# Optimization experiments

Measured on AMD Instinct MI355X. Metric: run time of the kernel, lower is better.

The kernel has to match this reference:

```python
import jax, jax.numpy as jnp
import numpy as np

EPS = 1e-5      # F.layer_norm default eps
ALPHA = 0.08    # ALALLaDA blend coefficient


def setup_inputs() -> dict:
    key = jax.random.key(0)
    ks = jax.random.split(key, 6)
    B, S, D, K = 2, 2048, 2048, 8
    Fh = D // 4
    h_L = jax.random.normal(ks[0], (B, S, D), jnp.float32)
    # nonzero -> masked position (stands in for input_ids == 126336)
    mask = jax.random.randint(ks[1], (B, S), 0, 2).astype(jnp.int32)
    Wr = jax.random.normal(ks[2], (K, D), jnp.float32) / np.sqrt(D).astype(np.float32)
    br = jnp.zeros((K,), jnp.float32)
    W1 = jax.random.normal(ks[3], (K, D, Fh), jnp.float32) / np.sqrt(D).astype(np.float32)
    b1 = jnp.zeros((K, Fh), jnp.float32)
    W2 = jax.random.normal(ks[4], (K, Fh, D), jnp.float32) / np.sqrt(Fh).astype(np.float32)
    b2 = jnp.zeros((K, D), jnp.float32)
    return {"h_L": h_L, "mask": mask, "Wr": Wr, "br": br,
            "W1": W1, "b1": b1, "W2": W2, "b2": b2, "range_r": 8}


def _router_blend(h_L, Wr, br, W1, b1, W2, b2, mask, range_r):
    B, S, D = h_L.shape
    masked = mask != 0
    um = (~masked).astype(h_L.dtype)  # unmasked validity [B,S]
    # Per-token, per-expert outputs M[b,s,k,d]: Linear -> exact GELU -> Linear.
    pre = jnp.einsum('bsd,kdf->bskf', h_L, W1) + b1
    M = jnp.einsum('bskf,kfd->bskd', jax.nn.gelu(pre, approximate=False), W2) + b2
    # Routing weights at every position (softmax over K experts).
    w = jax.nn.softmax(jnp.einsum('bsd,kd->bsk', h_L, Wr) + br, axis=-1)
    # Accumulate weighted expert outputs over the +/-range_r neighbor window,
    # counting only unmasked neighbors. Fixed small loop over 2r offsets.
    num = jnp.zeros((B, S, D), h_L.dtype)
    cnt = jnp.zeros((B, S), h_L.dtype)
    for o in range(-range_r, range_r + 1):
        if o == 0:
            continue
        if o > 0:  # neighbor t = a + o: shift left, zero-pad tail
            Mo = jnp.pad(M[:, o:], ((0, 0), (0, o), (0, 0), (0, 0)))
            vo = jnp.pad(um[:, o:], ((0, 0), (0, o)))
        else:      # neighbor t = a + o (o<0): shift right, zero-pad head
            Mo = jnp.pad(M[:, :o], ((0, 0), (-o, 0), (0, 0), (0, 0)))
            vo = jnp.pad(um[:, :o], ((0, 0), (-o, 0)))
        num = num + vo[..., None] * jnp.einsum('bsk,bskd->bsd', w, Mo)
        cnt = cnt + vo
    has = cnt > 0
    mean = num / jnp.maximum(cnt, 1.0)[..., None]   # mean over valid neighbors
    # layer_norm over d_model, no affine
    mu = mean.mean(-1, keepdims=True)
    var = jnp.mean((mean - mu) ** 2, axis=-1, keepdims=True)
    ln = (mean - mu) / jnp.sqrt(var + EPS)
    # delta is written only at masked positions that had >=1 neighbor
    delta = jnp.where((masked & has)[..., None], ln, 0.0)
    return h_L + ALPHA * delta


def reference(h_L, mask, Wr, br, W1, b1, W2, b2, range_r):
    return _router_blend(h_L, Wr, br, W1, b1, W2, b2, mask, range_r)
```

## Files before the change

### kernel.cpp

```cpp
#include <hip/hip_runtime.h>
#include <hip/hip_bf16.h>
#include <math.h>


#define ALPHA 0.08f
#define EPS 1e-5f

typedef __attribute__((ext_vector_type(8))) __bf16 bf16x8;
typedef __attribute__((ext_vector_type(8))) short short8;
typedef __attribute__((ext_vector_type(4))) float f32x4;

__device__ __forceinline__ unsigned short f2bf(float f) {
  unsigned u = __float_as_uint(f);
  u += 0x7fffu + ((u >> 16) & 1u);
  return (unsigned short)(u >> 16);
}
__device__ __forceinline__ float bf2f(unsigned short b) {
  return __uint_as_float(((unsigned)b) << 16);
}

#define GLD16(gptr, lptr)                                                     \
  __builtin_amdgcn_global_load_lds(                                           \
      (const __attribute__((address_space(1))) void*)(gptr),                  \
      (__attribute__((address_space(3))) void*)(lptr), 16, 0, 0)

__device__ __forceinline__ int wave_incl_scan(int v, int lane) {
#pragma unroll
  for (int off = 1; off < 64; off <<= 1) {
    int t = __shfl_up(v, off);
    if (lane >= off) v += t;
  }
  return v;
}

__global__ __launch_bounds__(1024) void scan_kernel(
    const int* __restrict__ mask, const int* __restrict__ rptr,
    int* __restrict__ ru, int* __restrict__ unm_idx,
    int* __restrict__ msk_idx, int* __restrict__ pos2row,
    int* __restrict__ counts) {
  __shared__ int sru[4097];
  __shared__ int wsum[16];
  __shared__ int wsum2[17];
  const int tid = threadIdx.x;
  const int lane = tid & 63, wv = tid >> 6;
  const int t0 = tid * 4;
  const int4 m4 = *(const int4*)(mask + t0);
  int f[4];
  f[0] = (m4.x == 0); f[1] = (m4.y == 0); f[2] = (m4.z == 0); f[3] = (m4.w == 0);
  const int tsum = f[0] + f[1] + f[2] + f[3];
  const int isc = wave_incl_scan(tsum, lane);
  if (lane == 63) wsum[wv] = isc;
  __syncthreads();
  if (tid == 0) {
    int acc = 0;
#pragma unroll
    for (int i = 0; i < 16; ++i) { int v = wsum[i]; wsum[i] = acc; acc += v; }
    sru[4096] = acc;
    counts[0] = acc;
    ru[4096] = acc;
  }
  __syncthreads();
  int ex = wsum[wv] + isc - tsum;
#pragma unroll
  for (int j = 0; j < 4; ++j) {
    sru[t0 + j] = ex;
    ru[t0 + j] = ex;
    if (f[j]) unm_idx[ex] = t0 + j;
    ex += f[j];
  }
  __syncthreads();
  const int r = rptr[0];
  int mval[4] = {m4.x, m4.y, m4.z, m4.w};
  int g[4];
#pragma unroll
  for (int j = 0; j < 4; ++j) {
    const int t = t0 + j;
    const int s = t & 2047, tb = t & ~2047;
    const int lo = max(s - r, 0), hi = min(s + r, 2047);
    const int cnt = sru[tb + hi + 1] - sru[tb + lo];
    g[j] = (mval[j] != 0 && cnt > 0) ? 1 : 0;
  }
  const int tsum2 = g[0] + g[1] + g[2] + g[3];
  const int isc2 = wave_incl_scan(tsum2, lane);
  if (lane == 63) wsum2[wv] = isc2;
  __syncthreads();
  if (tid == 0) {
    int acc = 0;
#pragma unroll
    for (int i = 0; i < 16; ++i) { int v = wsum2[i]; wsum2[i] = acc; acc += v; }
    counts[1] = acc;
  }
  __syncthreads();
  int ex2 = wsum2[wv] + isc2 - tsum2;
#pragma unroll
  for (int j = 0; j < 4; ++j) {
    const int t = t0 + j;
    pos2row[t] = g[j] ? ex2 : -1;
    if (g[j]) msk_idx[ex2] = t;
    ex2 += g[j];
  }
}

__global__ void packrouter_kernel(const float* __restrict__ h,
                                  const int* __restrict__ mask,
                                  const int* __restrict__ ru,
                                  const float* __restrict__ Wr,
                                  const float* __restrict__ br,
                                  float* __restrict__ w,
                                  unsigned short* __restrict__ hbc) {
  const int a = blockIdx.x;
  const int tid = threadIdx.x;
  const int lane = tid & 63, wid = tid >> 6;
  const size_t base = (size_t)a * 2048;
  const int d0 = tid * 8;
  float hv[8];
  *(float4*)(hv) = *(const float4*)(h + base + d0);
  *(float4*)(hv + 4) = *(const float4*)(h + base + d0 + 4);
  float acc[8];
#pragma unroll
  for (int k = 0; k < 8; ++k) {
    float wvv[8];
    *(float4*)(wvv) = *(const float4*)(Wr + (size_t)k * 2048 + d0);
    *(float4*)(wvv + 4) = *(const float4*)(Wr + (size_t)k * 2048 + d0 + 4);
    float s = 0.f;
#pragma unroll
    for (int j = 0; j < 8; ++j) s += hv[j] * wvv[j];
    acc[k] = s;
  }
#pragma unroll
  for (int off = 32; off > 0; off >>= 1)
#pragma unroll
    for (int k = 0; k < 8; ++k) acc[k] += __shfl_down(acc[k], off);
  __shared__ float red[4][8];
  __shared__ float logits[8];
  if (lane == 0)
#pragma unroll
    for (int k = 0; k < 8; ++k) red[wid][k] = acc[k];
  __syncthreads();
  if (tid < 8)
    logits[tid] = red[0][tid] + red[1][tid] + red[2][tid] + red[3][tid] + br[tid];
  __syncthreads();
  if (tid == 0) {
    float mx = logits[0];
#pragma unroll
    for (int k = 1; k < 8; ++k) mx = fmaxf(mx, logits[k]);
    float e[8], se = 0.f;
#pragma unroll
    for (int k = 0; k < 8; ++k) {
      e[k] = expf(logits[k] - mx);
      se += e[k];
    }
    const float is = 1.f / se;
#pragma unroll
    for (int k = 0; k < 8; ++k) w[(size_t)a * 8 + k] = e[k] * is;
  }
  if (mask[a] == 0) {
    const int i = ru[a];
    short8 o;
#pragma unroll
    for (int j = 0; j < 8; ++j) o[j] = (short)f2bf(hv[j]);
    *(short8*)(hbc + (size_t)i * 2048 + d0) = o;
  }
}

__global__ void transpose_pack_kernel(const float* __restrict__ src,
                                      unsigned short* __restrict__ dst,
                                      int R, int C, size_t dstStride,
                                      size_t dstExpStride) {
  __shared__ float tile[32][33];
  const int k = blockIdx.z;
  src += (size_t)k * (size_t)R * (size_t)C;
  dst += (size_t)k * dstExpStride;
  const int c0 = blockIdx.x * 32;
  const int r0 = blockIdx.y * 32;
  const int tx = threadIdx.x;
  const int ty = threadIdx.y;
#pragma unroll
  for (int i = 0; i < 4; ++i)
    tile[ty + 8 * i][tx] = src[(size_t)(r0 + ty + 8 * i) * C + (c0 + tx)];
  __syncthreads();
#pragma unroll
  for (int i = 0; i < 4; ++i) {
    const int c = c0 + ty + 8 * i;
    dst[(size_t)c * dstStride + (size_t)(r0 + tx)] = f2bf(tile[tx][ty + 8 * i]);
  }
}

template <int EPI>
__global__ __launch_bounds__(256, 2) void gemm_bt_kernel(
    const unsigned short* __restrict__ A, const unsigned short* __restrict__ Bt,
    float* __restrict__ Cf, unsigned short* __restrict__ Cb,
    const float* __restrict__ bias, const int* __restrict__ counts, int cidx,
    int N, int Kd) {
  const int Mlim = counts[cidx];
  const int bm = blockIdx.y * 128;
  if (bm >= Mlim) return;
  __shared__ __align__(16) unsigned short L[4][8192];
  const int tid = threadIdx.x;
  const int lane = tid & 63;
  const int wid = tid >> 6;
  const int bn = blockIdx.x * 128;
  const int wr = wid >> 1;
  const int wc = wid & 1;

  f32x4 acc[4][4];
#pragma unroll
  for (int m = 0; m < 4; ++m)
#pragma unroll
    for (int n = 0; n < 4; ++n) acc[m][n] = (f32x4){0.f, 0.f, 0.f, 0.f};

  const int srow = wid * 16 + (lane >> 2);
  const int scol = (lane & 3) * 8;
  const unsigned short* gA0 = A + (size_t)(bm + srow) * Kd + scol;
  const unsigned short* gA1 = gA0 + (size_t)64 * Kd;
  const unsigned short* gB0 = Bt + (size_t)(bn + srow) * Kd + scol;
  const unsigned short* gB1 = gB0 + (size_t)64 * Kd;

  const int aoff = (wr * 64 + (lane & 15)) * 32 + (lane >> 4) * 8;
  const int boff = (wc * 64 + (lane & 15)) * 32 + (lane >> 4) * 8;

#define STAGE(buf, t)                                                         \
  {                                                                           \
    const int k0_ = (t) << 5;                                                 \
    unsigned short* la_ = &L[(buf)][0] + wid * 512;                           \
    unsigned short* lb_ = &L[(buf)][4096] + wid * 512;                        \
    GLD16(gA0 + k0_, la_);                                                    \
    GLD16(gA1 + k0_, la_ + 2048);                                             \
    GLD16(gB0 + k0_, lb_);                                                    \
    GLD16(gB1 + k0_, lb_ + 2048);                                             \
  }

#define COMPUTE(buf)                                                          \
  {                                                                           \
    const unsigned short* As_ = &L[(buf)][0];                                 \
    const unsigned short* Bs_ = &L[(buf)][4096];                              \
    bf16x8 af[4], bfr[4];                                                     \
    _Pragma("unroll") for (int m = 0; m < 4; ++m) af[m] =                     \
        __builtin_bit_cast(bf16x8, *(const short8*)(As_ + aoff + m * 512));   \
    _Pragma("unroll") for (int n = 0; n < 4; ++n) bfr[n] =                    \
        __builtin_bit_cast(bf16x8, *(const short8*)(Bs_ + boff + n * 512));   \
    _Pragma("unroll") for (int m = 0; m < 4; ++m)                             \
        _Pragma("unroll") for (int n = 0; n < 4; ++n) acc[m][n] =             \
            __builtin_amdgcn_mfma_f32_16x16x32_bf16(af[m], bfr[n],            \
                                                    acc[m][n], 0, 0, 0);      \
  }

  const int nt = Kd >> 5;
  STAGE(0, 0);
  STAGE(1, 1);
  STAGE(2, 2);
#pragma unroll 1
  for (int t = 0; t < nt - 3; ++t) {
    asm volatile("s_waitcnt vmcnt(8)" ::: "memory");
    __builtin_amdgcn_s_barrier();
    __builtin_amdgcn_sched_barrier(0);
    STAGE((t + 3) & 3, t + 3);
    COMPUTE(t & 3);
  }
  {
    asm volatile("s_waitcnt vmcnt(8)" ::: "memory");
    __builtin_amdgcn_s_barrier();
    __builtin_amdgcn_sched_barrier(0);
    COMPUTE((nt - 3) & 3);
  }
  {
    asm volatile("s_waitcnt vmcnt(4)" ::: "memory");
    __builtin_amdgcn_s_barrier();
    __builtin_amdgcn_sched_barrier(0);
    COMPUTE((nt - 2) & 3);
  }
  {
    asm volatile("s_waitcnt vmcnt(0)" ::: "memory");
    __builtin_amdgcn_s_barrier();
    __builtin_amdgcn_sched_barrier(0);
    COMPUTE((nt - 1) & 3);
  }
#undef STAGE
#undef COMPUTE

  const int r0 = bm + wr * 64 + (lane >> 4) * 4;
  const int c0 = bn + wc * 64 + (lane & 15);
#pragma unroll
  for (int m = 0; m < 4; ++m) {
#pragma unroll
    for (int n = 0; n < 4; ++n) {
      const int col = c0 + n * 16;
#pragma unroll
      for (int i = 0; i < 4; ++i) {
        const int row = r0 + m * 16 + i;
        if (row >= Mlim) continue;
        const size_t off = (size_t)row * N + col;
        float v = acc[m][n][i];
        if (EPI == 1) {
          v += bias[col];
          v = 0.5f * v * (1.0f + erff(v * 0.70710678118654752f));
          Cb[off] = f2bf(v);
        } else {
          Cf[off] = v;
        }
      }
    }
  }
}

__global__ void window_kernel(const unsigned short* __restrict__ Act_c,
                              const float* __restrict__ w,
                              const int* __restrict__ msk_idx,
                              const int* __restrict__ ru,
                              const int* __restrict__ rptr,
                              const int* __restrict__ counts,
                              unsigned short* __restrict__ G_c) {
  const int i = blockIdx.y;
  if (i >= counts[1]) return;
  const int a = msk_idx[i];
  const int s = a & 2047;
  const int tb = a & ~2047;
  const int r = rptr[0];
  const int lo = max(s - r, 0), hi = min(s + r, 2047);
  const int jlo = ru[tb + lo], jhi = ru[tb + hi + 1];
  const int c = blockIdx.x * 2048 + threadIdx.x * 8;
  float acc[8] = {0.f, 0.f, 0.f, 0.f, 0.f, 0.f, 0.f, 0.f};
  for (int j = jlo; j < jhi; ++j) {
    const short8 v = *(const short8*)(Act_c + (size_t)j * 4096 + c);
#pragma unroll
    for (int jj = 0; jj < 8; ++jj) acc[jj] += bf2f((unsigned short)v[jj]);
  }
  const float wv = w[(size_t)a * 8 + (c >> 9)];
  short8 o8;
#pragma unroll
  for (int jj = 0; jj < 8; ++jj) o8[jj] = (short)f2bf(acc[jj] * wv);
  *(short8*)(G_c + (size_t)i * 4096 + c) = o8;
}

__global__ void final_kernel(const float* __restrict__ h,
                             const int* __restrict__ pos2row,
                             const float* __restrict__ w,
                             const float* __restrict__ b2,
                             const float* __restrict__ num_c,
                             const int* __restrict__ ru,
                             const int* __restrict__ rptr,
                             float* __restrict__ out) {
  const int a = blockIdx.x;
  const int tid = threadIdx.x;
  const int lane = tid & 63, wid = tid >> 6;
  const size_t base = (size_t)a * 2048;
  const int d0 = tid * 8;
  const int row = pos2row[a];
  if (row < 0) {
    const float4 x0 = *(const float4*)(h + base + d0);
    const float4 x1 = *(const float4*)(h + base + d0 + 4);
    *(float4*)(out + base + d0) = x0;
    *(float4*)(out + base + d0 + 4) = x1;
    return;
  }
  const int s = a & 2047;
  const int tb = a & ~2047;
  const int r = rptr[0];
  const int lo = max(s - r, 0), hi = min(s + r, 2047);
  const int cnt = ru[tb + hi + 1] - ru[tb + lo];
  float wk[8];
#pragma unroll
  for (int k = 0; k < 8; ++k) wk[k] = w[(size_t)a * 8 + k];
  const float cntf = (float)cnt;
  const float icnt = 1.0f / cntf;
  float mval[8];
  float s1 = 0.f, s2 = 0.f;
#pragma unroll
  for (int j = 0; j < 8; ++j) {
    const int d = d0 + j;
    float wb2 = 0.f;
#pragma unroll
    for (int k = 0; k < 8; ++k) wb2 += wk[k] * b2[(size_t)k * 2048 + d];
    const float v = (num_c[(size_t)row * 2048 + d] + cntf * wb2) * icnt;
    mval[j] = v;
    s1 += v;
    s2 += v * v;
  }
#pragma unroll
  for (int off = 32; off > 0; off >>= 1) {
    s1 += __shfl_down(s1, off);
    s2 += __shfl_down(s2, off);
  }
  __shared__ float red[8];
  if (lane == 0) {
    red[wid] = s1;
    red[4 + wid] = s2;
  }
  __syncthreads();
  const float S1 = red[0] + red[1] + red[2] + red[3];
  const float S2 = red[4] + red[5] + red[6] + red[7];
  const float mu = S1 * (1.0f / 2048.0f);
  const float var = S2 * (1.0f / 2048.0f) - mu * mu;
  const float rin = rsqrtf(var + EPS);
#pragma unroll
  for (int j = 0; j < 8; ++j) {
    const int d = d0 + j;
    out[base + d] = h[base + d] + ALPHA * ((mval[j] - mu) * rin);
  }
}

extern "C" void kernel_launch(void* const* d_in, const int* in_sizes, int n_in,
                              void* d_out, int out_size, void* d_ws,
                              size_t ws_size, hipStream_t stream) {
  const float* h = (const float*)d_in[0];
  const int* mask = (const int*)d_in[1];
  const float* Wr = (const float*)d_in[2];
  const float* br = (const float*)d_in[3];
  const float* W1 = (const float*)d_in[4];
  const float* b1 = (const float*)d_in[5];
  const float* W2 = (const float*)d_in[6];
  const float* b2 = (const float*)d_in[7];
  const int* rptr = (const int*)d_in[8];
  float* out = (float*)d_out;

  char* ws = (char*)d_ws;
  unsigned short* hbc = (unsigned short*)(ws + 0);
  unsigned short* B1t = (unsigned short*)(ws + 16777216);
  unsigned short* B2t = (unsigned short*)(ws + 33554432);
  unsigned short* Act_c = (unsigned short*)(ws + 50331648);
  unsigned short* G_c = (unsigned short*)(ws + 83886080);
  float* num_c = (float*)(ws + 50331648);
  float* wbuf = (float*)(ws + 117440512);
  int* ru = (int*)(ws + 117571584);
  int* unm_idx = ru + 4100;
  int* msk_idx = unm_idx + 4096;
  int* pos2row = msk_idx + 4096;
  int* counts = pos2row + 4096;

  scan_kernel<<<1, 1024, 0, stream>>>(mask, rptr, ru, unm_idx, msk_idx,
                                      pos2row, counts);
  packrouter_kernel<<<4096, 256, 0, stream>>>(h, mask, ru, Wr, br, wbuf, hbc);
  transpose_pack_kernel<<<dim3(16, 64, 8), dim3(32, 8), 0, stream>>>(
      W1, B1t, 2048, 512, 2048, (size_t)512 * 2048);
  transpose_pack_kernel<<<dim3(64, 16, 8), dim3(32, 8), 0, stream>>>(
      W2, B2t, 512, 2048, 4096, 512);
  gemm_bt_kernel<1><<<dim3(32, 32), 256, 0, stream>>>(
      hbc, B1t, nullptr, Act_c, b1, counts, 0, 4096, 2048);
  window_kernel<<<dim3(2, 4096), 256, 0, stream>>>(Act_c, wbuf, msk_idx, ru,
                                                   rptr, counts, G_c);
  gemm_bt_kernel<0><<<dim3(16, 32), 256, 0, stream>>>(
      G_c, B2t, num_c, nullptr, nullptr, counts, 1, 2048, 4096);
  final_kernel<<<4096, 256, 0, stream>>>(h, pos2row, wbuf, b2, num_c, ru,
                                         rptr, out);
}
```

Baseline: 346.7 us.

## Deepen GEMM prefetch to 5 LDS stages, swizzle workgroups, merge weight transpose kernels

The GEMM kernel moves from a 4-buffer to a 5-buffer LDS ring with four tiles in flight, adjusting the vmcnt waits to match. Workgroup IDs are remapped with an XCD-style swizzle so that neighbouring tiles share L2 on the same die. The two weight transpose/pack launches are merged into one launch of 16384 blocks. The extra LDS (80KB per block) may cut occupancy below the launch_bounds target of 2 blocks per CU, and the swizzle makes early-exit blocks for masked-out rows scattered rather than contiguous.

```diff
diff --git a/kernel.cpp b/kernel.cpp
--- a/kernel.cpp
+++ b/kernel.cpp
@@ -163,16 +163,32 @@
   }
 }
 
-__global__ void transpose_pack_kernel(const float* __restrict__ src,
-                                      unsigned short* __restrict__ dst,
-                                      int R, int C, size_t dstStride,
-                                      size_t dstExpStride) {
+__global__ void tpack_kernel(const float* __restrict__ W1,
+                             const float* __restrict__ W2,
+                             unsigned short* __restrict__ B1t,
+                             unsigned short* __restrict__ B2t) {
   __shared__ float tile[32][33];
-  const int k = blockIdx.z;
-  src += (size_t)k * (size_t)R * (size_t)C;
-  dst += (size_t)k * dstExpStride;
-  const int c0 = blockIdx.x * 32;
-  const int r0 = blockIdx.y * 32;
+  int id = blockIdx.x;
+  const float* src;
+  unsigned short* dst;
+  int C, c0, r0;
+  size_t dstStride;
+  if (id < 8192) {
+    const int k = id >> 10, rem = id & 1023;
+    const int cblk = rem >> 6, rblk = rem & 63;
+    src = W1 + (size_t)k * 2048 * 512;
+    dst = B1t + (size_t)k * 512 * 2048;
+    C = 512; dstStride = 2048;
+    c0 = cblk * 32; r0 = rblk * 32;
+  } else {
+    id -= 8192;
+    const int k = id >> 10, rem = id & 1023;
+    const int cblk = rem >> 4, rblk = rem & 15;
+    src = W2 + (size_t)k * 512 * 2048;
+    dst = B2t + (size_t)k * 512;
+    C = 2048; dstStride = 4096;
+    c0 = cblk * 32; r0 = rblk * 32;
+  }
   const int tx = threadIdx.x;
   const int ty = threadIdx.y;
 #pragma unroll
@@ -192,14 +208,19 @@
     float* __restrict__ Cf, unsigned short* __restrict__ Cb,
     const float* __restrict__ bias, const int* __restrict__ counts, int cidx,
     int N, int Kd) {
+  const int gx = gridDim.x, gy = gridDim.y;
+  const int nwg = gx * gy;
+  const int o = blockIdx.y * gx + blockIdx.x;
+  const int q = nwg >> 3;
+  const int swz = (o & 7) * q + (o >> 3);
+  const int bn = (swz / gy) * 128;
+  const int bm = (swz % gy) * 128;
   const int Mlim = counts[cidx];
-  const int bm = blockIdx.y * 128;
   if (bm >= Mlim) return;
-  __shared__ __align__(16) unsigned short L[4][8192];
+  __shared__ __align__(16) unsigned short L[5][8192];
   const int tid = threadIdx.x;
   const int lane = tid & 63;
   const int wid = tid >> 6;
-  const int bn = blockIdx.x * 128;
   const int wr = wid >> 1;
   const int wc = wid & 1;
 
@@ -249,31 +270,44 @@
   STAGE(0, 0);
   STAGE(1, 1);
   STAGE(2, 2);
+  STAGE(3, 3);
+  int cb = 0, sb = 4;
 #pragma unroll 1
-  for (int t = 0; t < nt - 3; ++t) {
-    asm volatile("s_waitcnt vmcnt(8)" ::: "memory");
+  for (int t = 0; t < nt - 4; ++t) {
+    asm volatile("s_waitcnt vmcnt(12)" ::: "memory");
     __builtin_amdgcn_s_barrier();
     __builtin_amdgcn_sched_barrier(0);
-    STAGE((t + 3) & 3, t + 3);
-    COMPUTE(t & 3);
+    STAGE(sb, t + 4);
+    COMPUTE(cb);
+    cb = (cb == 4) ? 0 : cb + 1;
+    sb = (sb == 4) ? 0 : sb + 1;
+  }
+  {
+    asm volatile("s_waitcnt vmcnt(12)" ::: "memory");
+    __builtin_amdgcn_s_barrier();
+    __builtin_amdgcn_sched_barrier(0);
+    COMPUTE(cb);
+    cb = (cb == 4) ? 0 : cb + 1;
   }
   {
     asm volatile("s_waitcnt vmcnt(8)" ::: "memory");
     __builtin_amdgcn_s_barrier();
     __builtin_amdgcn_sched_barrier(0);
-    COMPUTE((nt - 3) & 3);
+    COMPUTE(cb);
+    cb = (cb == 4) ? 0 : cb + 1;
   }
   {
     asm volatile("s_waitcnt vmcnt(4)" ::: "memory");
     __builtin_amdgcn_s_barrier();
     __builtin_amdgcn_sched_barrier(0);
-    COMPUTE((nt - 2) & 3);
+    COMPUTE(cb);
+    cb = (cb == 4) ? 0 : cb + 1;
   }
   {
     asm volatile("s_waitcnt vmcnt(0)" ::: "memory");
     __builtin_amdgcn_s_barrier();
     __builtin_amdgcn_sched_barrier(0);
-    COMPUTE((nt - 1) & 3);
+    COMPUTE(cb);
   }
 #undef STAGE
 #undef COMPUTE
@@ -430,10 +464,7 @@
   scan_kernel<<<1, 1024, 0, stream>>>(mask, rptr, ru, unm_idx, msk_idx,
                                       pos2row, counts);
   packrouter_kernel<<<4096, 256, 0, stream>>>(h, mask, ru, Wr, br, wbuf, hbc);
-  transpose_pack_kernel<<<dim3(16, 64, 8), dim3(32, 8), 0, stream>>>(
-      W1, B1t, 2048, 512, 2048, (size_t)512 * 2048);
-  transpose_pack_kernel<<<dim3(64, 16, 8), dim3(32, 8), 0, stream>>>(
-      W2, B2t, 512, 2048, 4096, 512);
+  tpack_kernel<<<16384, dim3(32, 8), 0, stream>>>(W1, W2, B1t, B2t);
   gemm_bt_kernel<1><<<dim3(32, 32), 256, 0, stream>>>(
       hbc, B1t, nullptr, Act_c, b1, counts, 0, 4096, 2048);
   window_kernel<<<dim3(2, 4096), 256, 0, stream>>>(Act_c, wbuf, msk_idx, ru,
```

After: 347.0 us. Within noise of the previous version (+0.1%).
